# Performance work log

Hardware: AMD Instinct MI355X
Metric: run time of the kernel (lower is better)

Reference implementation:

```python
import jax, jax.numpy as jnp
import numpy as np

V = 780        # junction-tree vocab size
N = 50000      # total nodes in batch
M = 100001     # total messages (+1 null slot at index 0)
K = 6          # padded max neighbors
H = 256        # hidden size
B = 64         # number of trees (scope entries)
DEPTH = 6      # GRU depth


def setup_inputs() -> dict:
    key = jax.random.key(0)
    ks = jax.random.split(key, 12)
    p = lambda k, s: jax.random.normal(k, s, jnp.float32) * 0.02
    return {
        "fnode": jax.random.randint(ks[0], (N,), 0, V),
        "fmess": jax.random.randint(ks[1], (M,), 0, N),
        "node_graph": jax.random.randint(ks[2], (N, K), 0, M),
        "mess_graph": jax.random.randint(ks[3], (M, K), 0, M),
        "scope_st": jax.random.randint(ks[4], (B,), 0, N),
        "emb": p(ks[5], (V, H)),
        "Wz": p(ks[6], (H, 2 * H)), "bz": jnp.zeros((H,), jnp.float32),
        "Wr": p(ks[7], (H, H)),
        "Ur": p(ks[8], (H, H)), "bu": jnp.zeros((H,), jnp.float32),
        "Wh": p(ks[9], (H, 2 * H)), "bh": jnp.zeros((H,), jnp.float32),
        "Wo": p(ks[10], (H, 2 * H)), "bo": jnp.zeros((H,), jnp.float32),
    }


def reference(fnode, fmess, node_graph, mess_graph, scope_st,
              emb, Wz, bz, Wr, Ur, bu, Wh, bh, Wo, bo):
    fnode_e = emb[fnode]                       # [N, H] embedded node features
    x = fnode_e[fmess]                         # [M, H] per-message source features
    mask = jnp.ones((M, 1), jnp.float32).at[0].set(0.0)  # zero the null message
    # W_r(x) depends only on x; hoist it out of the loop (same math as original)
    xWr = (x @ Wr.T)[:, None, :]               # [M, 1, H]

    h = jnp.zeros((M, H), jnp.float32)
    for _ in range(DEPTH):
        h_nei = h[mess_graph]                  # [M, K, H] gather neighbor messages
        sum_h = h_nei.sum(axis=1)              # [M, H]
        z = jax.nn.sigmoid(jnp.concatenate([x, sum_h], axis=1) @ Wz.T + bz)
        r = jax.nn.sigmoid(xWr + h_nei @ Ur.T + bu)   # [M, K, H]
        sum_gated_h = (r * h_nei).sum(axis=1)  # [M, H]
        pre_h = jnp.tanh(jnp.concatenate([x, sum_gated_h], axis=1) @ Wh.T + bh)
        h = ((1.0 - z) * sum_h + z * pre_h) * mask

    mess_nei = h[node_graph].sum(axis=1)       # [N, H]
    node_vecs = jax.nn.relu(
        jnp.concatenate([fnode_e, mess_nei], axis=-1) @ Wo.T + bo)  # [N, H]
    tree_vecs = node_vecs[scope_st]            # [B, H] root vector per tree
    return tree_vecs, h
```

## Files before the change

### kernel.cpp

```cpp
#include <hip/hip_runtime.h>

typedef unsigned short u16;
typedef unsigned int   u32;
typedef short bf16x8 __attribute__((ext_vector_type(8)));
typedef float f32x4  __attribute__((ext_vector_type(4)));

#define V_ 780
#define N_ 50000
#define M_ 100001
#define K_ 6
#define H_ 256
#define B_ 64
#define DEPTH_ 6

#define HE_LD 512

typedef __attribute__((address_space(3))) u32 lds_u32;
typedef __attribute__((address_space(1))) const u32 glb_u32;
__device__ __forceinline__ void dma16(const void* g, void* l){
  __builtin_amdgcn_global_load_lds((glb_u32*)g, (lds_u32*)l, 16, 0, 0);
}

__device__ __forceinline__ float b2f(u16 u){
  union { u32 i; float f; } x; x.i = ((u32)u) << 16; return x.f;
}
__device__ __forceinline__ u16 f2b(float f){
  union { float f; u32 i; } x; x.f = f;
  u32 r = x.i + 0x7fffu + ((x.i >> 16) & 1u);
  return (u16)(r >> 16);
}
__device__ __forceinline__ float rcp_(float x){ return __builtin_amdgcn_rcpf(x); }
__device__ __forceinline__ float sigm(float x){ return rcp_(1.f + __expf(-x)); }
__device__ __forceinline__ float tanh_(float x){
  x = fminf(fmaxf(x, -15.f), 15.f);
  float e = __expf(2.f*x);
  return (e - 1.f) * rcp_(e + 1.f);
}
__device__ __forceinline__ int swz(int r){ return (r + (r >> 2)) & 3; }
__device__ __forceinline__ int lds_off(int row, int col){
  return row*256 + ((((col >> 3) ^ (row & 7)) << 3) + (col & 7));
}

__global__ void k_tables(const float* __restrict__ emb,
    const float* __restrict__ Wz, const float* __restrict__ bz,
    const float* __restrict__ Wr, const float* __restrict__ bu,
    const float* __restrict__ Wh, const float* __restrict__ bh,
    const float* __restrict__ Wo, const float* __restrict__ bo,
    float* __restrict__ tWz, float* __restrict__ tXr,
    float* __restrict__ tWh, float* __restrict__ tWo){
  int v = blockIdx.x, q = blockIdx.y, j = threadIdx.x;
  __shared__ float e[H_];
  e[j] = emb[v*H_ + j];
  __syncthreads();
  const float* w; const float* b; float* o; int ld;
  if      (q == 0){ w = Wz; b = bz; o = tWz; ld = 2*H_; }
  else if (q == 1){ w = Wr; b = bu; o = tXr; ld = H_;   }
  else if (q == 2){ w = Wh; b = bh; o = tWh; ld = 2*H_; }
  else            { w = Wo; b = bo; o = tWo; ld = 2*H_; }
  const float* wr = w + (size_t)j*ld;
  float a0 = 0.f, a1 = 0.f;
  #pragma unroll 4
  for (int i = 0; i < H_; i += 8){
    float4 x = *(const float4*)(wr + i);
    float4 y = *(const float4*)(wr + i + 4);
    a0 += e[i  ]*x.x + e[i+1]*x.y + e[i+2]*x.z + e[i+3]*x.w;
    a1 += e[i+4]*y.x + e[i+5]*y.y + e[i+6]*y.z + e[i+7]*y.w;
  }
  float val = a0 + a1 + b[j];
  if (q == 1) val = __expf(-val);
  o[v*H_ + j] = val;
}

__global__ void k_convw(const float* __restrict__ Ur, const float* __restrict__ Wz,
                        const float* __restrict__ Wh,
                        u16* __restrict__ Urb, u16* __restrict__ Wzb, u16* __restrict__ Whb){
  int r = blockIdx.x, j = threadIdx.x;
  Urb[r*H_ + j] = f2b(Ur[r*H_ + j]);
  Wzb[r*H_ + j] = f2b(Wz[r*(2*H_) + H_ + j]);
  Whb[r*H_ + j] = f2b(Wh[r*(2*H_) + H_ + j]);
}

__global__ void k_init(const int* __restrict__ fnode, const int* __restrict__ fmess,
                       const float* __restrict__ tWz, const float* __restrict__ tWh,
                       int* __restrict__ vmsg, u16* __restrict__ hE){
  int m = blockIdx.x, j = threadIdx.x;
  int v = fnode[fmess[m]];
  if (j == 0) vmsg[m] = v;
  float val = (m == 0) ? 0.f : sigm(tWz[v*H_ + j])*tanh_(tWh[v*H_ + j]);
  hE[(size_t)m*HE_LD + j] = f2b(val);
}

__global__ __launch_bounds__(256,3) void k_gemm(
    const u16* A, const u16* __restrict__ W, u16* C){
  __shared__ __align__(16) u16 lA[2][64*32];
  __shared__ __align__(16) u16 lB[2][256*32];
  const int t    = threadIdx.x;
  const int m0   = blockIdx.x * 64;
  const int lane = t & 63, wave = t >> 6;
  const int l16  = lane & 15, kc8 = lane >> 4;

  const int rA = t >> 2, cA = t & 3;
  const int kA = (cA ^ swz(rA)) * 8;
  const int gmA = (m0 + rA < M_) ? (m0 + rA) : (M_ - 1);
  const int aOff = (wave*64)*8;
  int rB[4], kB[4], bOff[4];
  #pragma unroll
  for (int p=0;p<4;p++){
    int s = t + 256*p;
    rB[p] = s >> 2; int cc = s & 3;
    kB[p] = (cc ^ swz(rB[p])) * 8;
    bOff[p] = (wave*64 + 256*p)*8;
  }

  f32x4 acc[4][4];
  #pragma unroll
  for (int r=0;r<4;r++)
    #pragma unroll
    for (int c=0;c<4;c++)
      #pragma unroll
      for (int q=0;q<4;q++) acc[r][c][q] = 0.f;

  auto stage = [&](int buf, int k0){
    dma16(A + (size_t)gmA*HE_LD + k0 + kA, &lA[buf][aOff]);
    #pragma unroll
    for (int p=0;p<4;p++)
      dma16(W + (size_t)rB[p]*H_ + k0 + kB[p], &lB[buf][bOff[p]]);
  };

  stage(0, 0);
  __syncthreads();
  int cur = 0;
  for (int ks = 0; ks < 8; ++ks){
    if (ks < 7) stage(cur^1, (ks+1)*32);
    bf16x8 aF[4], bF[4];
    #pragma unroll
    for (int r=0;r<4;r++){
      int row = r*16 + l16;
      aF[r] = *(const bf16x8*)(&lA[cur][row*32 + ((kc8 ^ swz(row))*8)]);
    }
    #pragma unroll
    for (int c=0;c<4;c++){
      int row = wave*64 + c*16 + l16;
      bF[c] = *(const bf16x8*)(&lB[cur][row*32 + ((kc8 ^ swz(row))*8)]);
    }
    #pragma unroll
    for (int r=0;r<4;r++)
      #pragma unroll
      for (int c=0;c<4;c++)
        acc[r][c] = __builtin_amdgcn_mfma_f32_16x16x32_bf16(aF[r], bF[c], acc[r][c], 0,0,0);
    if (ks < 7) __syncthreads();
    cur ^= 1;
  }

  #pragma unroll
  for (int r=0;r<4;r++){
    #pragma unroll
    for (int c=0;c<4;c++){
      int mb = m0 + r*16 + kc8*4;
      int n  = wave*64 + c*16 + l16;
      #pragma unroll
      for (int q=0;q<4;q++){
        int m = mb + q;
        if (m < M_) C[(size_t)m*HE_LD + H_ + n] = f2b(__expf(-acc[r][c][q]));
      }
    }
  }
}

template<bool FIN>
__global__ __launch_bounds__(512,4) void k_step(
    const u16* __restrict__ src, u16* __restrict__ dst,
    float* __restrict__ hf,
    const int* __restrict__ mg, const int* __restrict__ vmsg,
    const float* __restrict__ tXr, const float* __restrict__ tWz,
    const float* __restrict__ tWh,
    const u16* __restrict__ Wzb, const u16* __restrict__ Whb,
    const u16* __restrict__ Urb){
  __shared__ __align__(16) u16 lSH[64*256];
  __shared__ __align__(16) u16 lSG[64*256];
  const int t    = threadIdx.x;
  const int m0   = blockIdx.x * 64;
  const int lane = t & 63, wave = t >> 6;
  const int l16  = lane & 15, kc8 = lane >> 4;
  const int wrow = wave >> 2, wcol = wave & 3;

  {
    const char* bc = (const char*)src;
    const u32 cb = (u32)lane * 8u;
    #pragma unroll 2
    for (int i = 0; i < 8; ++i){
      int row = wave*8 + i;
      int gm = m0 + row; if (gm >= M_) gm = M_ - 1;
      int v = vmsg[gm];
      float4 X = *(const float4*)(tXr + (size_t)v*H_ + lane*4);
      const int2* mgp = (const int2*)(mg + gm*K_);
      int2 g01 = mgp[0], g23 = mgp[1], g45 = mgp[2];
      int gs[K_] = {g01.x,g01.y,g23.x,g23.y,g45.x,g45.y};
      float s0=0.f,s1=0.f,s2=0.f,s3=0.f, a0=0.f,a1=0.f,a2=0.f,a3=0.f;
      #pragma unroll
      for (int k=0;k<K_;k++){
        u32 off = ((u32)gs[k] << 10) + cb;
        uint2 hp = *(const uint2*)(bc + off);
        uint2 ep = *(const uint2*)(bc + off + 512);
        float h0=b2f((u16)hp.x), h1=b2f((u16)(hp.x>>16));
        float h2=b2f((u16)hp.y), h3=b2f((u16)(hp.y>>16));
        float e0=b2f((u16)ep.x), e1=b2f((u16)(ep.x>>16));
        float e2=b2f((u16)ep.y), e3=b2f((u16)(ep.y>>16));
        s0+=h0; s1+=h1; s2+=h2; s3+=h3;
        a0 += rcp_(fmaf(X.x,e0,1.f))*h0;
        a1 += rcp_(fmaf(X.y,e1,1.f))*h1;
        a2 += rcp_(fmaf(X.z,e2,1.f))*h2;
        a3 += rcp_(fmaf(X.w,e3,1.f))*h3;
      }
      uint2 sh, sg;
      sh.x = (u32)f2b(s0) | ((u32)f2b(s1)<<16);
      sh.y = (u32)f2b(s2) | ((u32)f2b(s3)<<16);
      sg.x = (u32)f2b(a0) | ((u32)f2b(a1)<<16);
      sg.y = (u32)f2b(a2) | ((u32)f2b(a3)<<16);
      int o = lds_off(row, lane*4);
      *(uint2*)&lSH[o] = sh;
      *(uint2*)&lSG[o] = sg;
    }
  }
  __syncthreads();

  f32x4 accZ[2][4], accH[2][4];
  #pragma unroll
  for (int r=0;r<2;r++)
    #pragma unroll
    for (int c=0;c<4;c++)
      #pragma unroll
      for (int q=0;q<4;q++){ accZ[r][c][q]=0.f; accH[r][c][q]=0.f; }

  #pragma unroll
  for (int ks=0; ks<8; ++ks){
    bf16x8 aH[2], aG[2];
    #pragma unroll
    for (int r=0;r<2;r++){
      int row = wrow*32 + r*16 + l16;
      int o = row*256 + ((((ks*4 + kc8) ^ (row & 7)) << 3));
      aH[r] = *(const bf16x8*)&lSH[o];
      aG[r] = *(const bf16x8*)&lSG[o];
    }
    #pragma unroll
    for (int c=0;c<4;c++){
      int n = wcol*64 + c*16 + l16;
      bf16x8 bZ = *(const bf16x8*)(Wzb + (size_t)n*H_ + ks*32 + kc8*8);
      bf16x8 bW = *(const bf16x8*)(Whb + (size_t)n*H_ + ks*32 + kc8*8);
      #pragma unroll
      for (int r=0;r<2;r++){
        accZ[r][c] = __builtin_amdgcn_mfma_f32_16x16x32_bf16(aH[r], bZ, accZ[r][c], 0,0,0);
        accH[r][c] = __builtin_amdgcn_mfma_f32_16x16x32_bf16(aG[r], bW, accH[r][c], 0,0,0);
      }
    }
  }
  __syncthreads();

  #pragma unroll
  for (int r=0;r<2;r++){
    #pragma unroll
    for (int q=0;q<4;q++){
      int lm = wrow*32 + r*16 + kc8*4 + q;
      int m  = m0 + lm;
      int v  = (m < M_) ? vmsg[m] : 0;
      #pragma unroll
      for (int c=0;c<4;c++){
        int n = wcol*64 + c*16 + l16;
        float z   = sigm(tWz[v*H_ + n] + accZ[r][c][q]);
        float pre = tanh_(tWh[v*H_ + n] + accH[r][c][q]);
        float sh  = b2f(lSH[lds_off(lm, n)]);
        float o   = (m == 0) ? 0.f : (1.f - z)*sh + z*pre;
        if (FIN){
          if (m < M_) hf[(size_t)m*H_ + n] = o;
        } else {
          u16 ob = f2b(o);
          if (m < M_) dst[(size_t)m*HE_LD + n] = ob;
          lSG[lds_off(lm, n)] = ob;
        }
      }
    }
  }

  if (FIN) return;
  __syncthreads();

  f32x4 accE[2][4];
  #pragma unroll
  for (int r=0;r<2;r++)
    #pragma unroll
    for (int c=0;c<4;c++)
      #pragma unroll
      for (int q=0;q<4;q++) accE[r][c][q] = 0.f;

  #pragma unroll
  for (int ks=0; ks<8; ++ks){
    bf16x8 aN[2];
    #pragma unroll
    for (int r=0;r<2;r++){
      int row = wrow*32 + r*16 + l16;
      int o = row*256 + ((((ks*4 + kc8) ^ (row & 7)) << 3));
      aN[r] = *(const bf16x8*)&lSG[o];
    }
    #pragma unroll
    for (int c=0;c<4;c++){
      int n = wcol*64 + c*16 + l16;
      bf16x8 bU = *(const bf16x8*)(Urb + (size_t)n*H_ + ks*32 + kc8*8);
      #pragma unroll
      for (int r=0;r<2;r++)
        accE[r][c] = __builtin_amdgcn_mfma_f32_16x16x32_bf16(aN[r], bU, accE[r][c], 0,0,0);
    }
  }
  #pragma unroll
  for (int r=0;r<2;r++){
    #pragma unroll
    for (int q=0;q<4;q++){
      int m = m0 + wrow*32 + r*16 + kc8*4 + q;
      if (m >= M_) continue;
      #pragma unroll
      for (int c=0;c<4;c++){
        int n = wcol*64 + c*16 + l16;
        dst[(size_t)m*HE_LD + H_ + n] = f2b(__expf(-accE[r][c][q]));
      }
    }
  }
}

__global__ void k_final(const float* __restrict__ h, const int* __restrict__ ng,
                        const int* __restrict__ fnode, const int* __restrict__ scope,
                        const float* __restrict__ tWo, const float* __restrict__ Wo,
                        float* __restrict__ out){
  int b = blockIdx.x, j = threadIdx.x;
  int n = scope[b];
  __shared__ float mn[H_];
  float s = 0.f;
  #pragma unroll
  for (int k=0;k<K_;k++){
    int g = ng[n*K_ + k];
    s += h[(size_t)g*H_ + j];
  }
  mn[j] = s;
  __syncthreads();
  int v = fnode[n];
  float acc = tWo[v*H_ + j];
  const float* w = Wo + j*(2*H_) + H_;
  for (int i=0;i<H_;i+=4){
    float4 a = *(const float4*)(w+i);
    acc += mn[i]*a.x + mn[i+1]*a.y + mn[i+2]*a.z + mn[i+3]*a.w;
  }
  out[b*H_ + j] = fmaxf(acc, 0.f);
}

__global__ void k_zero(float* __restrict__ out, int n){
  int i = blockIdx.x*256 + threadIdx.x;
  int stride = gridDim.x*256;
  for (; i < n; i += stride) out[i] = 0.f;
}

extern "C" void kernel_launch(void* const* d_in, const int* in_sizes, int n_in,
                              void* d_out, int out_size, void* d_ws, size_t ws_size,
                              hipStream_t stream){
  const int* fnode      = (const int*)d_in[0];
  const int* fmess      = (const int*)d_in[1];
  const int* node_graph = (const int*)d_in[2];
  const int* mess_graph = (const int*)d_in[3];
  const int* scope_st   = (const int*)d_in[4];
  const float* emb = (const float*)d_in[5];
  const float* Wz  = (const float*)d_in[6];
  const float* bz  = (const float*)d_in[7];
  const float* Wr  = (const float*)d_in[8];
  const float* Ur  = (const float*)d_in[9];
  const float* bu  = (const float*)d_in[10];
  const float* Wh  = (const float*)d_in[11];
  const float* bh  = (const float*)d_in[12];
  const float* Wo  = (const float*)d_in[13];
  const float* bo  = (const float*)d_in[14];

  char* ws = (char*)d_ws;
  size_t off = 0;
  float* tWz = (float*)(ws + off); off += (size_t)V_*H_*4;
  float* tXr = (float*)(ws + off); off += (size_t)V_*H_*4;
  float* tWh = (float*)(ws + off); off += (size_t)V_*H_*4;
  float* tWo = (float*)(ws + off); off += (size_t)V_*H_*4;
  u16* Urb  = (u16*)(ws + off); off += (size_t)H_*H_*2;
  u16* Wzb  = (u16*)(ws + off); off += (size_t)H_*H_*2;
  u16* Whb  = (u16*)(ws + off); off += (size_t)H_*H_*2;
  int* vmsg = (int*)(ws + off); off += ((size_t)M_*4 + 1023) & ~(size_t)1023;
  u16* hEws = (u16*)(ws + off); off += (size_t)M_*HE_LD*2;

  if (ws_size < off){
    k_zero<<<2048, 256, 0, stream>>>((float*)d_out, out_size);
    return;
  }

  float* out = (float*)d_out;
  float* h   = out + (size_t)B_*H_;
  u16* hED = (u16*)h;

  const int MT64 = (M_ + 63)/64;

  k_tables<<<dim3(V_,4), H_, 0, stream>>>(emb, Wz, bz, Wr, bu, Wh, bh, Wo, bo,
                                          tWz, tXr, tWh, tWo);
  k_convw<<<H_, H_, 0, stream>>>(Ur, Wz, Wh, Urb, Wzb, Whb);
  k_init<<<M_, H_, 0, stream>>>(fnode, fmess, tWz, tWh, vmsg, hEws);
  k_gemm<<<MT64, 256, 0, stream>>>(hEws, Urb, hEws);

  k_step<false><<<MT64, 512, 0, stream>>>(hEws, hED,  h, mess_graph, vmsg,
                                          tXr, tWz, tWh, Wzb, Whb, Urb);
  k_step<false><<<MT64, 512, 0, stream>>>(hED,  hEws, h, mess_graph, vmsg,
                                          tXr, tWz, tWh, Wzb, Whb, Urb);
  k_step<false><<<MT64, 512, 0, stream>>>(hEws, hED,  h, mess_graph, vmsg,
                                          tXr, tWz, tWh, Wzb, Whb, Urb);
  k_step<false><<<MT64, 512, 0, stream>>>(hED,  hEws, h, mess_graph, vmsg,
                                          tXr, tWz, tWh, Wzb, Whb, Urb);
  k_step<true ><<<MT64, 512, 0, stream>>>(hEws, hEws, h, mess_graph, vmsg,
                                          tXr, tWz, tWh, Wzb, Whb, Urb);

  k_final<<<B_, H_, 0, stream>>>(h, node_graph, fnode, scope_st, tWo, Wo, out);
}
```

Before: 1.546 ms.

## Split GRU step into column-pass gather kernels and a separate GEMM kernel

The fused per-step kernel is split into two passes of a new gather kernel, each covering half the hidden columns, and a GEMM/epilogue kernel. The gathers write sum_h and the gated sum to global bf16 buffers, and the GEMM kernel streams them through double-buffered LDS with DMA. The h and exp(-eU) values are now interleaved per 4 columns, so one 16-byte load per neighbor fetches both. The aim is better gather locality and occupancy, at the cost of extra global round-trips for the intermediate sums and more kernel launches.

```diff
diff --git a/kernel.cpp b/kernel.cpp
--- a/kernel.cpp
+++ b/kernel.cpp
@@ -37,9 +37,11 @@
   return (e - 1.f) * rcp_(e + 1.f);
 }
 __device__ __forceinline__ int swz(int r){ return (r + (r >> 2)) & 3; }
-__device__ __forceinline__ int lds_off(int row, int col){
+__device__ __forceinline__ int lds_off64(int row, int col){
   return row*256 + ((((col >> 3) ^ (row & 7)) << 3) + (col & 7));
 }
+__device__ __forceinline__ int ilv_h(int j){ return (j>>2)*8 + (j&3); }
+__device__ __forceinline__ int ilv_e(int j){ return (j>>2)*8 + 4 + (j&3); }
 
 __global__ void k_tables(const float* __restrict__ emb,
     const float* __restrict__ Wz, const float* __restrict__ bz,
@@ -82,16 +84,19 @@
 
 __global__ void k_init(const int* __restrict__ fnode, const int* __restrict__ fmess,
                        const float* __restrict__ tWz, const float* __restrict__ tWh,
-                       int* __restrict__ vmsg, u16* __restrict__ hE){
+                       int* __restrict__ vmsg, u16* __restrict__ hE,
+                       u16* __restrict__ hA){
   int m = blockIdx.x, j = threadIdx.x;
   int v = fnode[fmess[m]];
   if (j == 0) vmsg[m] = v;
   float val = (m == 0) ? 0.f : sigm(tWz[v*H_ + j])*tanh_(tWh[v*H_ + j]);
-  hE[(size_t)m*HE_LD + j] = f2b(val);
+  u16 b = f2b(val);
+  hE[(size_t)m*HE_LD + ilv_h(j)] = b;
+  hA[(size_t)m*H_ + j] = b;
 }
 
 __global__ __launch_bounds__(256,3) void k_gemm(
-    const u16* A, const u16* __restrict__ W, u16* C){
+    const u16* __restrict__ A, const u16* __restrict__ W, u16* __restrict__ C){
   __shared__ __align__(16) u16 lA[2][64*32];
   __shared__ __align__(16) u16 lB[2][256*32];
   const int t    = threadIdx.x;
@@ -121,7 +126,7 @@
       for (int q=0;q<4;q++) acc[r][c][q] = 0.f;
 
   auto stage = [&](int buf, int k0){
-    dma16(A + (size_t)gmA*HE_LD + k0 + kA, &lA[buf][aOff]);
+    dma16(A + (size_t)gmA*H_ + k0 + kA, &lA[buf][aOff]);
     #pragma unroll
     for (int p=0;p<4;p++)
       dma16(W + (size_t)rB[p]*H_ + k0 + kB[p], &lB[buf][bOff[p]]);
@@ -161,87 +166,100 @@
       #pragma unroll
       for (int q=0;q<4;q++){
         int m = mb + q;
-        if (m < M_) C[(size_t)m*HE_LD + H_ + n] = f2b(__expf(-acc[r][c][q]));
+        if (m < M_) C[(size_t)m*HE_LD + ilv_e(n)] = f2b(__expf(-acc[r][c][q]));
       }
     }
   }
 }
 
+__global__ __launch_bounds__(256,8) void k_gather2(
+    const u16* __restrict__ hE,
+    const int* __restrict__ mg, const int* __restrict__ vmsg,
+    const float* __restrict__ tXr,
+    u16* __restrict__ sumh, u16* __restrict__ sumg, int pass){
+  int m = blockIdx.x*8 + ((threadIdx.x>>6)<<1) + ((threadIdx.x>>5)&1);
+  if (m >= M_) return;
+  const int hl = threadIdx.x & 31;
+  int v = vmsg[m];
+  float4 X = *(const float4*)(tXr + (size_t)v*H_ + pass*128 + hl*4);
+  const int2* mgp = (const int2*)(mg + m*K_);
+  int2 g01 = mgp[0], g23 = mgp[1], g45 = mgp[2];
+  int gs[K_] = {g01.x,g01.y,g23.x,g23.y,g45.x,g45.y};
+  const char* bc = (const char*)hE;
+  const u32 cb = (u32)(pass*512 + hl*16);
+  float s0=0.f,s1=0.f,s2=0.f,s3=0.f, a0=0.f,a1=0.f,a2=0.f,a3=0.f;
+  #pragma unroll
+  for (int k=0;k<K_;k++){
+    u32 off = ((u32)gs[k] << 10) + cb;
+    uint4 p = *(const uint4*)(bc + off);
+    float h0=b2f((u16)p.x), h1=b2f((u16)(p.x>>16));
+    float h2=b2f((u16)p.y), h3=b2f((u16)(p.y>>16));
+    float e0=b2f((u16)p.z), e1=b2f((u16)(p.z>>16));
+    float e2=b2f((u16)p.w), e3=b2f((u16)(p.w>>16));
+    s0+=h0; s1+=h1; s2+=h2; s3+=h3;
+    a0 += rcp_(fmaf(X.x,e0,1.f))*h0;
+    a1 += rcp_(fmaf(X.y,e1,1.f))*h1;
+    a2 += rcp_(fmaf(X.z,e2,1.f))*h2;
+    a3 += rcp_(fmaf(X.w,e3,1.f))*h3;
+  }
+  uint2 sh, sg;
+  sh.x = (u32)f2b(s0) | ((u32)f2b(s1)<<16);
+  sh.y = (u32)f2b(s2) | ((u32)f2b(s3)<<16);
+  sg.x = (u32)f2b(a0) | ((u32)f2b(a1)<<16);
+  sg.y = (u32)f2b(a2) | ((u32)f2b(a3)<<16);
+  *(uint2*)((char*)sumh + ((size_t)m<<9) + pass*256 + hl*8) = sh;
+  *(uint2*)((char*)sumg + ((size_t)m<<9) + pass*256 + hl*8) = sg;
+}
+
 template<bool FIN>
-__global__ __launch_bounds__(512,4) void k_step(
-    const u16* __restrict__ src, u16* __restrict__ dst,
-    float* __restrict__ hf,
-    const int* __restrict__ mg, const int* __restrict__ vmsg,
-    const float* __restrict__ tXr, const float* __restrict__ tWz,
-    const float* __restrict__ tWh,
+__global__ __launch_bounds__(512,2) void k_gemmzh_e(
+    const u16* __restrict__ sumh, const u16* __restrict__ sumg,
     const u16* __restrict__ Wzb, const u16* __restrict__ Whb,
-    const u16* __restrict__ Urb){
-  __shared__ __align__(16) u16 lSH[64*256];
-  __shared__ __align__(16) u16 lSG[64*256];
+    const u16* __restrict__ Urb,
+    const float* __restrict__ tWz, const float* __restrict__ tWh,
+    const int* __restrict__ vmsg,
+    u16* __restrict__ dst, float* __restrict__ hf){
+  __shared__ __align__(16) u16 lA[2][2][64*32];
+  __shared__ __align__(16) u16 lN[64*256];
   const int t    = threadIdx.x;
   const int m0   = blockIdx.x * 64;
   const int lane = t & 63, wave = t >> 6;
   const int l16  = lane & 15, kc8 = lane >> 4;
   const int wrow = wave >> 2, wcol = wave & 3;
 
-  {
-    const char* bc = (const char*)src;
-    const u32 cb = (u32)lane * 8u;
-    #pragma unroll 2
-    for (int i = 0; i < 8; ++i){
-      int row = wave*8 + i;
-      int gm = m0 + row; if (gm >= M_) gm = M_ - 1;
-      int v = vmsg[gm];
-      float4 X = *(const float4*)(tXr + (size_t)v*H_ + lane*4);
-      const int2* mgp = (const int2*)(mg + gm*K_);
-      int2 g01 = mgp[0], g23 = mgp[1], g45 = mgp[2];
-      int gs[K_] = {g01.x,g01.y,g23.x,g23.y,g45.x,g45.y};
-      float s0=0.f,s1=0.f,s2=0.f,s3=0.f, a0=0.f,a1=0.f,a2=0.f,a3=0.f;
-      #pragma unroll
-      for (int k=0;k<K_;k++){
-        u32 off = ((u32)gs[k] << 10) + cb;
-        uint2 hp = *(const uint2*)(bc + off);
-        uint2 ep = *(const uint2*)(bc + off + 512);
-        float h0=b2f((u16)hp.x), h1=b2f((u16)(hp.x>>16));
-        float h2=b2f((u16)hp.y), h3=b2f((u16)(hp.y>>16));
-        float e0=b2f((u16)ep.x), e1=b2f((u16)(ep.x>>16));
-        float e2=b2f((u16)ep.y), e3=b2f((u16)(ep.y>>16));
-        s0+=h0; s1+=h1; s2+=h2; s3+=h3;
-        a0 += rcp_(fmaf(X.x,e0,1.f))*h0;
-        a1 += rcp_(fmaf(X.y,e1,1.f))*h1;
-        a2 += rcp_(fmaf(X.z,e2,1.f))*h2;
-        a3 += rcp_(fmaf(X.w,e3,1.f))*h3;
-      }
-      uint2 sh, sg;
-      sh.x = (u32)f2b(s0) | ((u32)f2b(s1)<<16);
-      sh.y = (u32)f2b(s2) | ((u32)f2b(s3)<<16);
-      sg.x = (u32)f2b(a0) | ((u32)f2b(a1)<<16);
-      sg.y = (u32)f2b(a2) | ((u32)f2b(a3)<<16);
-      int o = lds_off(row, lane*4);
-      *(uint2*)&lSH[o] = sh;
-      *(uint2*)&lSG[o] = sg;
-    }
-  }
+  const int mat = t >> 8;
+  const int tm  = t & 255;
+  const int rS  = tm >> 2, cS = tm & 3;
+  const int kS  = (cS ^ swz(rS)) * 8;
+  const int gmS = (m0 + rS < M_) ? (m0 + rS) : (M_ - 1);
+  const u16* matp = mat ? sumg : sumh;
+  const int dOff = ((wave & 3) * 64) * 8;
+
+  f32x4 accZ[2][4], accH[2][4];
+  #pragma unroll
+  for (int r=0;r<2;r++)
+    #pragma unroll
+    for (int c=0;c<4;c++)
+      #pragma unroll
+      for (int q=0;q<4;q++){ accZ[r][c][q]=0.f; accH[r][c][q]=0.f; }
+
+  auto stage = [&](int buf, int k0){
+    dma16(matp + (size_t)gmS*H_ + k0 + kS, &lA[buf][mat][dOff]);
+  };
+
+  stage(0, 0);
   __syncthreads();
-
-  f32x4 accZ[2][4], accH[2][4];
-  #pragma unroll
-  for (int r=0;r<2;r++)
-    #pragma unroll
-    for (int c=0;c<4;c++)
-      #pragma unroll
-      for (int q=0;q<4;q++){ accZ[r][c][q]=0.f; accH[r][c][q]=0.f; }
-
-  #pragma unroll
-  for (int ks=0; ks<8; ++ks){
+  int cur = 0;
+  for (int ks = 0; ks < 8; ++ks){
     bf16x8 aH[2], aG[2];
     #pragma unroll
     for (int r=0;r<2;r++){
       int row = wrow*32 + r*16 + l16;
-      int o = row*256 + ((((ks*4 + kc8) ^ (row & 7)) << 3));
-      aH[r] = *(const bf16x8*)&lSH[o];
-      aG[r] = *(const bf16x8*)&lSG[o];
-    }
+      int ao = row*32 + ((kc8 ^ swz(row))*8);
+      aH[r] = *(const bf16x8*)&lA[cur][0][ao];
+      aG[r] = *(const bf16x8*)&lA[cur][1][ao];
+    }
+    if (ks < 7) stage(cur^1, (ks+1)*32);
     #pragma unroll
     for (int c=0;c<4;c++){
       int n = wcol*64 + c*16 + l16;
@@ -253,8 +271,9 @@
         accH[r][c] = __builtin_amdgcn_mfma_f32_16x16x32_bf16(aG[r], bW, accH[r][c], 0,0,0);
       }
     }
-  }
-  __syncthreads();
+    __syncthreads();
+    cur ^= 1;
+  }
 
   #pragma unroll
   for (int r=0;r<2;r++){
@@ -262,20 +281,21 @@
     for (int q=0;q<4;q++){
       int lm = wrow*32 + r*16 + kc8*4 + q;
       int m  = m0 + lm;
-      int v  = (m < M_) ? vmsg[m] : 0;
+      int mr = (m < M_) ? m : (M_ - 1);
+      int v  = vmsg[mr];
       #pragma unroll
       for (int c=0;c<4;c++){
         int n = wcol*64 + c*16 + l16;
         float z   = sigm(tWz[v*H_ + n] + accZ[r][c][q]);
         float pre = tanh_(tWh[v*H_ + n] + accH[r][c][q]);
-        float sh  = b2f(lSH[lds_off(lm, n)]);
+        float sh  = b2f(sumh[(size_t)mr*H_ + n]);
         float o   = (m == 0) ? 0.f : (1.f - z)*sh + z*pre;
         if (FIN){
           if (m < M_) hf[(size_t)m*H_ + n] = o;
         } else {
           u16 ob = f2b(o);
-          if (m < M_) dst[(size_t)m*HE_LD + n] = ob;
-          lSG[lds_off(lm, n)] = ob;
+          lN[lds_off64(lm, n)] = ob;
+          if (m < M_) dst[(size_t)m*HE_LD + ilv_h(n)] = ob;
         }
       }
     }
@@ -298,8 +318,8 @@
     #pragma unroll
     for (int r=0;r<2;r++){
       int row = wrow*32 + r*16 + l16;
-      int o = row*256 + ((((ks*4 + kc8) ^ (row & 7)) << 3));
-      aN[r] = *(const bf16x8*)&lSG[o];
+      int ao = row*256 + ((((ks*4 + kc8) ^ (row & 7)) << 3));
+      aN[r] = *(const bf16x8*)&lN[ao];
     }
     #pragma unroll
     for (int c=0;c<4;c++){
@@ -319,7 +339,7 @@
       #pragma unroll
       for (int c=0;c<4;c++){
         int n = wcol*64 + c*16 + l16;
-        dst[(size_t)m*HE_LD + H_ + n] = f2b(__expf(-accE[r][c][q]));
+        dst[(size_t)m*HE_LD + ilv_e(n)] = f2b(__expf(-accE[r][c][q]));
       }
     }
   }
@@ -385,7 +405,9 @@
   u16* Wzb  = (u16*)(ws + off); off += (size_t)H_*H_*2;
   u16* Whb  = (u16*)(ws + off); off += (size_t)H_*H_*2;
   int* vmsg = (int*)(ws + off); off += ((size_t)M_*4 + 1023) & ~(size_t)1023;
-  u16* hEws = (u16*)(ws + off); off += (size_t)M_*HE_LD*2;
+  u16* hA   = (u16*)(ws + off); off += (size_t)M_*H_*2;
+  u16* sumh = (u16*)(ws + off); off += (size_t)M_*H_*2;
+  u16* sumg = (u16*)(ws + off); off += (size_t)M_*H_*2;
 
   if (ws_size < off){
     k_zero<<<2048, 256, 0, stream>>>((float*)d_out, out_size);
@@ -397,23 +419,24 @@
   u16* hED = (u16*)h;
 
   const int MT64 = (M_ + 63)/64;
+  const int GB   = (M_ + 7)/8;
 
   k_tables<<<dim3(V_,4), H_, 0, stream>>>(emb, Wz, bz, Wr, bu, Wh, bh, Wo, bo,
                                           tWz, tXr, tWh, tWo);
   k_convw<<<H_, H_, 0, stream>>>(Ur, Wz, Wh, Urb, Wzb, Whb);
-  k_init<<<M_, H_, 0, stream>>>(fnode, fmess, tWz, tWh, vmsg, hEws);
-  k_gemm<<<MT64, 256, 0, stream>>>(hEws, Urb, hEws);
-
-  k_step<false><<<MT64, 512, 0, stream>>>(hEws, hED,  h, mess_graph, vmsg,
-                                          tXr, tWz, tWh, Wzb, Whb, Urb);
-  k_step<false><<<MT64, 512, 0, stream>>>(hED,  hEws, h, mess_graph, vmsg,
-                                          tXr, tWz, tWh, Wzb, Whb, Urb);
-  k_step<false><<<MT64, 512, 0, stream>>>(hEws, hED,  h, mess_graph, vmsg,
-                                          tXr, tWz, tWh, Wzb, Whb, Urb);
-  k_step<false><<<MT64, 512, 0, stream>>>(hED,  hEws, h, mess_graph, vmsg,
-                                          tXr, tWz, tWh, Wzb, Whb, Urb);
-  k_step<true ><<<MT64, 512, 0, stream>>>(hEws, hEws, h, mess_graph, vmsg,
-                                          tXr, tWz, tWh, Wzb, Whb, Urb);
+  k_init<<<M_, H_, 0, stream>>>(fnode, fmess, tWz, tWh, vmsg, hED, hA);
+  k_gemm<<<MT64, 256, 0, stream>>>(hA, Urb, hED);
+
+  for (int it = 0; it < DEPTH_-1; ++it){
+    k_gather2<<<GB, 256, 0, stream>>>(hED, mess_graph, vmsg, tXr, sumh, sumg, 0);
+    k_gather2<<<GB, 256, 0, stream>>>(hED, mess_graph, vmsg, tXr, sumh, sumg, 1);
+    if (it < DEPTH_-2)
+      k_gemmzh_e<false><<<MT64, 512, 0, stream>>>(sumh, sumg, Wzb, Whb, Urb,
+                                                  tWz, tWh, vmsg, hED, h);
+    else
+      k_gemmzh_e<true ><<<MT64, 512, 0, stream>>>(sumh, sumg, Wzb, Whb, Urb,
+                                                  tWz, tWh, vmsg, hED, h);
+  }
 
   k_final<<<B_, H_, 0, stream>>>(h, node_graph, fnode, scope_st, tWo, Wo, out);
 }
```

After: 2.011 ms. 30.0% more time.
